# Kernel tuning notes

Measured on AMD Instinct MI355X. Metric: run time of the kernel, lower is better.

The kernel has to match this reference:

```python
import jax, jax.numpy as jnp
import numpy as np

N_NODES = 100000
N_EDGES = 600000
D = 128
NUM_RELS = 200


def setup_inputs() -> dict:
    key = jax.random.key(0)
    ks = jax.random.split(key, 12)
    s = 1.0 / np.sqrt(D)
    return {
        "h": jax.random.normal(ks[0], (N_NODES, D), jnp.float32),
        "prev_h": jax.random.normal(ks[1], (N_NODES, D), jnp.float32),
        "emb_rel": jax.random.normal(ks[2], (NUM_RELS, D), jnp.float32),
        "norm": jax.random.uniform(ks[3], (N_NODES, 1), jnp.float32),
        "weight_neighbor": jax.random.normal(ks[4], (D, D), jnp.float32) * s,
        "loop_weight": jax.random.normal(ks[5], (D, D), jnp.float32) * s,
        "evolve_loop_weight": jax.random.normal(ks[6], (D, D), jnp.float32) * s,
        "skip_connect_weight": jax.random.normal(ks[7], (D, D), jnp.float32) * s,
        "skip_connect_bias": jnp.zeros((D,), jnp.float32),
        "src": jax.random.randint(ks[8], (N_EDGES,), 0, N_NODES, jnp.int64),
        "dst": jax.random.randint(ks[9], (N_EDGES,), 0, N_NODES, jnp.int64),
        "etype": jax.random.randint(ks[10], (N_EDGES,), 0, NUM_RELS, jnp.int64),
    }


def reference(h, prev_h, emb_rel, norm, weight_neighbor, loop_weight,
              evolve_loop_weight, skip_connect_weight, skip_connect_bias,
              src, dst, etype):
    n = h.shape[0]
    # self-loop message: nodes with in-degree > 0 use loop_weight, else evolve_loop_weight
    in_deg = jax.ops.segment_sum(jnp.ones_like(dst, dtype=jnp.float32), dst,
                                 num_segments=n)  # [N]
    loop_message = jnp.where(in_deg[:, None] > 0,
                             h @ loop_weight,
                             h @ evolve_loop_weight)  # [N, D]
    # skip gate from previous layer hidden state
    skip_weight = jax.nn.sigmoid(prev_h @ skip_connect_weight + skip_connect_bias)
    # msg_func: gather src node feats + relation embedding, per-edge GEMM
    msg = (h[src] + emb_rel[etype]) @ weight_neighbor  # [E, D]
    # fn.sum scatter aggregation, then apply_func: multiply by node norm
    agg = jax.ops.segment_sum(msg, dst, num_segments=n)  # [N, D]
    node_repr = agg * norm
    # skip_connect (prev_h non-empty) + self_loop branch
    node_repr = node_repr + loop_message
    node_repr = skip_weight * node_repr + (1.0 - skip_weight) * prev_h
    # activation
    return jax.nn.relu(node_repr)
```

## Files before the change

kernel.cpp:

```cpp
#include <hip/hip_runtime.h>

#define DD 128

typedef __attribute__((ext_vector_type(8))) short short8;
typedef __attribute__((ext_vector_type(4))) float f32x4;
typedef __attribute__((ext_vector_type(4))) int i32x4;

__device__ __forceinline__ unsigned short f2bf(float f) {
    union { float f; unsigned int i; } c; c.f = f;
    unsigned int x = c.i;
    return (unsigned short)((x + 0x7fffu + ((x >> 16) & 1u)) >> 16);
}
__device__ __forceinline__ float bfu(unsigned short u) {
    union { unsigned int i; float f; } c; c.i = ((unsigned int)u) << 16; return c.f;
}
__device__ __forceinline__ void gload_lds16(const void* g, void* l) {
    __builtin_amdgcn_global_load_lds(
        (const __attribute__((address_space(1))) unsigned int*)g,
        (__attribute__((address_space(3))) unsigned int*)l, 16, 0, 0);
}
__device__ __forceinline__ int idx_at(const int* p, int e, int is64) {
    return is64 ? p[2 * e] : p[e];
}
__device__ __forceinline__ int block_is64(const int* dst, int nE, int* s_flag) {
    if (threadIdx.x == 0) *s_flag = 0;
    __syncthreads();
    int w = 2 * (int)threadIdx.x + 1;
    if (threadIdx.x < 128 && w < nE && dst[w] != 0) atomicOr(s_flag, 1);
    __syncthreads();
    return !*s_flag;
}

__global__ __launch_bounds__(256) void prep_k(
    const float* __restrict__ h,
    const float* __restrict__ W0, const float* __restrict__ W1,
    const float* __restrict__ W2, const float* __restrict__ emb,
    const int* __restrict__ dst,
    unsigned short* __restrict__ hB,
    unsigned short* __restrict__ embB, unsigned short* __restrict__ Wt,
    int* __restrict__ deg, int nN, int nEmbEl, int nE) {
    int tid = threadIdx.x;
    int bid = blockIdx.x;
    int nHistB = (nE + 1023) / 1024;
    if (bid < nHistB) {
        __shared__ int s_flag;
        int is64 = block_is64(dst, nE, &s_flag);
        int e0 = bid * 1024 + tid * 4;
        #pragma unroll
        for (int j = 0; j < 4; ++j) {
            int e = e0 + j;
            if (e < nE) atomicAdd(deg + idx_at(dst, e, is64), 1);
        }
        return;
    }
    bid -= nHistB;
    int totalH = nN * DD;
    int nConvH = (totalH + 8191) / 8192;
    if (bid < nConvH) {
        int base0 = bid * 8192;
        if (base0 + 8192 <= totalH) {
            int base = base0 + tid * 8;
            f32x4 x[4][2];
            #pragma unroll
            for (int i = 0; i < 4; ++i) {
                x[i][0] = *(const f32x4*)(h + base + i * 2048);
                x[i][1] = *(const f32x4*)(h + base + i * 2048 + 4);
            }
            #pragma unroll
            for (int i = 0; i < 4; ++i) {
                short8 p;
                #pragma unroll
                for (int j = 0; j < 4; ++j) {
                    p[j]     = (short)f2bf(x[i][0][j]);
                    p[4 + j] = (short)f2bf(x[i][1][j]);
                }
                *(short8*)(hB + base + i * 2048) = p;
            }
        } else {
            #pragma unroll
            for (int i = 0; i < 4; ++i) {
                int b2 = base0 + i * 2048 + tid * 8;
                if (b2 + 8 <= totalH) {
                    f32x4 x0 = *(const f32x4*)(h + b2);
                    f32x4 x1 = *(const f32x4*)(h + b2 + 4);
                    short8 p;
                    #pragma unroll
                    for (int j = 0; j < 4; ++j) {
                        p[j]     = (short)f2bf(x0[j]);
                        p[4 + j] = (short)f2bf(x1[j]);
                    }
                    *(short8*)(hB + b2) = p;
                } else {
                    for (int j = b2; j < totalH && j < b2 + 8; ++j)
                        hB[j] = f2bf(h[j]);
                }
            }
        }
        return;
    }
    bid -= nConvH;
    if (bid < 48) {
        const float* Ws[3] = {W0, W1, W2};
        int w = bid >> 4, chunk = bid & 15;
        unsigned short* T = Wt + w * (DD * DD);
        #pragma unroll
        for (int i = 0; i < 4; ++i) {
            int t = chunk * 1024 + i * 256 + tid;
            int n = t >> 7, k = t & 127;
            T[t] = f2bf(Ws[w][k * DD + n]);
        }
        return;
    }
    bid -= 48;
    int base = bid * 2048 + tid * 8;
    if (base + 8 <= nEmbEl) {
        f32x4 x0 = *(const f32x4*)(emb + base);
        f32x4 x1 = *(const f32x4*)(emb + base + 4);
        short8 p;
        #pragma unroll
        for (int j = 0; j < 4; ++j) {
            p[j]     = (short)f2bf(x0[j]);
            p[4 + j] = (short)f2bf(x1[j]);
        }
        *(short8*)(embB + base) = p;
    } else {
        for (int j = base; j < nEmbEl; ++j) embB[j] = f2bf(emb[j]);
    }
}

__global__ __launch_bounds__(1024) void scan1_k(const int* deg, int* off, int* bsum,
                                                int nN) {
    __shared__ int s[1024];
    int t = threadIdx.x, i = blockIdx.x * 1024 + t;
    int v = (i < nN) ? deg[i] : 0;
    s[t] = v;
    __syncthreads();
    for (int d = 1; d < 1024; d <<= 1) {
        int x = (t >= d) ? s[t - d] : 0;
        __syncthreads();
        s[t] += x;
        __syncthreads();
    }
    if (i < nN) off[i] = s[t] - v;
    if (t == 1023) bsum[blockIdx.x] = s[1023];
}

__global__ __launch_bounds__(1024) void scan23_k(const int* bsum, int* off,
                                                 int* cursor, int nN, int nB) {
    __shared__ int s[1024];
    int t = threadIdx.x;
    s[t] = (t < nB) ? bsum[t] : 0;
    __syncthreads();
    for (int d = 1; d < 1024; d <<= 1) {
        int x = (t >= d) ? s[t - d] : 0;
        __syncthreads();
        s[t] += x;
        __syncthreads();
    }
    int base = (blockIdx.x == 0) ? 0 : s[blockIdx.x - 1];
    int i = blockIdx.x * 1024 + t;
    if (i < nN) {
        int o = off[i] + base;
        off[i] = o;
        cursor[i] = o;
    }
}

__global__ __launch_bounds__(256) void sort_k(const int* src, const int* dst,
                                              const int* et, int nE,
                                              int* cursor, unsigned int* edges) {
    __shared__ int s_flag;
    int is64 = block_is64(dst, nE, &s_flag);
    int e = blockIdx.x * 256 + threadIdx.x;
    if (e >= nE) return;
    int d = idx_at(dst, e, is64);
    int pos = atomicAdd(cursor + d, 1);
    edges[pos] = (unsigned int)idx_at(src, e, is64) |
                 ((unsigned int)idx_at(et, e, is64) << 17);
}

__global__ __launch_bounds__(256) void gather_k(
    const unsigned short* __restrict__ hB, const unsigned short* __restrict__ embB,
    const unsigned int* __restrict__ edges, const int* __restrict__ off,
    const int* __restrict__ deg, const float* __restrict__ normv,
    char* __restrict__ aggP, int nN) {
    int lane = threadIdx.x & 63;
    int v = blockIdx.x * 4 + (threadIdx.x >> 6);
    if (v >= nN) return;
    int slot = lane >> 4, l16 = lane & 15;
    int b = off[v], n = deg[v];
    float a[8] = {0.f, 0.f, 0.f, 0.f, 0.f, 0.f, 0.f, 0.f};
    for (int base = 0; base < n; base += 8) {
        int m0 = base + slot, m1 = base + 4 + slot;
        bool v0 = m0 < n, v1 = m1 < n;
        unsigned int w0 = 0, w1 = 0;
        if (v0) w0 = edges[b + m0];
        if (v1) w1 = edges[b + m1];
        short8 hv0, rv0, hv1, rv1;
        if (v0) {
            hv0 = *(const short8*)(hB + (size_t)(w0 & 0x1FFFFu) * DD + l16 * 8);
            rv0 = *(const short8*)(embB + (size_t)(w0 >> 17) * DD + l16 * 8);
        }
        if (v1) {
            hv1 = *(const short8*)(hB + (size_t)(w1 & 0x1FFFFu) * DD + l16 * 8);
            rv1 = *(const short8*)(embB + (size_t)(w1 >> 17) * DD + l16 * 8);
        }
        if (v0) {
            #pragma unroll
            for (int j = 0; j < 8; ++j)
                a[j] += bfu((unsigned short)hv0[j]) + bfu((unsigned short)rv0[j]);
        }
        if (v1) {
            #pragma unroll
            for (int j = 0; j < 8; ++j)
                a[j] += bfu((unsigned short)hv1[j]) + bfu((unsigned short)rv1[j]);
        }
    }
    #pragma unroll
    for (int j = 0; j < 8; ++j) {
        a[j] += __shfl_xor(a[j], 16);
        a[j] += __shfl_xor(a[j], 32);
    }
    if (slot == 0) {
        float nm = normv[v];
        short8 p;
        #pragma unroll
        for (int j = 0; j < 8; ++j) p[j] = (short)f2bf(a[j] * nm);
        *(short8*)(aggP + (size_t)v * 512 + l16 * 16) = p;
    }
}

__global__ __launch_bounds__(256, 3) void fused_k(
    const unsigned short* __restrict__ hB,
    const float* __restrict__ prevh,
    const float* __restrict__ bias,
    const char* __restrict__ aggP,
    const unsigned short* __restrict__ Wt,
    float* __restrict__ out, int nN) {
    __shared__ unsigned short lds[3 * 64 * 128];
    const int lane = threadIdx.x & 63;
    const int wv = threadIdx.x >> 6;
    const int q = lane >> 4, cl = lane & 15;
    const int node_base = blockIdx.x * 64;
    const int ncb = wv * 32;

    {
        int r0 = lane >> 4;
        int c  = lane & 15;
        #pragma unroll
        for (int it = 0; it < 4; ++it) {
            int r = it * 16 + wv * 4 + r0;
            int row = node_base + r; if (row > nN - 1) row = nN - 1;
            int sw = (c ^ (r & 15)) << 4;
            char* base = (char*)lds + (it * 16 + wv * 4) * 256;
            gload_lds16(aggP + (size_t)row * 512 + sw, base);
            gload_lds16((const char*)hB + (size_t)row * 256 + sw, base + 16384);
        }
    }
    {
        f32x4 t0[4], t1[4];
        #pragma unroll
        for (int it = 0; it < 4; ++it) {
            int pos = it * 512 + lane * 8;
            int row = pos >> 7;
            int col = pos & 127;
            int node = node_base + wv * 16 + row;
            if (node > nN - 1) node = nN - 1;
            const float* g = prevh + (size_t)node * DD + col;
            t0[it] = *(const f32x4*)g;
            t1[it] = *(const f32x4*)(g + 4);
        }
        #pragma unroll
        for (int it = 0; it < 4; ++it) {
            int pos = it * 512 + lane * 8;
            int r = wv * 16 + (pos >> 7);
            int c = (pos & 127) >> 3;
            short8 p;
            #pragma unroll
            for (int j = 0; j < 4; ++j) {
                p[j]     = (short)f2bf(t0[it][j]);
                p[4 + j] = (short)f2bf(t1[it][j]);
            }
            *(short8*)((char*)lds + 32768 + r * 256 + ((c ^ (r & 15)) << 4)) = p;
        }
    }
    __syncthreads();

    const unsigned short* lA = lds;
    const unsigned short* lH = lds + 64 * 128;
    const unsigned short* lP = lds + 2 * 64 * 128;

    f32x4 accM[4][2], accG[4][2];
    #pragma unroll
    for (int mt = 0; mt < 4; ++mt)
        #pragma unroll
        for (int nt = 0; nt < 2; ++nt) {
            accM[mt][nt] = (f32x4){0.f, 0.f, 0.f, 0.f};
            accG[mt][nt] = (f32x4){0.f, 0.f, 0.f, 0.f};
        }

    #pragma unroll
    for (int ks = 0; ks < 4; ++ks) {
        short8 bn[2], bl[2], bs[2];
        #pragma unroll
        for (int nt = 0; nt < 2; ++nt) {
            int n = (ncb + nt * 16 + cl) * DD + ks * 32 + q * 8;
            bn[nt] = *(const short8*)(Wt + n);
            bl[nt] = *(const short8*)(Wt + DD * DD + n);
            bs[nt] = *(const short8*)(Wt + 2 * DD * DD + n);
        }
        int swz = ((ks * 4 + q) ^ cl) << 3;
        #pragma unroll
        for (int mt = 0; mt < 4; ++mt) {
            int off = (mt * 16 + cl) * 128 + swz;
            short8 aA = *(const short8*)(lA + off);
            short8 aH = *(const short8*)(lH + off);
            short8 aP = *(const short8*)(lP + off);
            #pragma unroll
            for (int nt = 0; nt < 2; ++nt) {
                accM[mt][nt] = __builtin_amdgcn_mfma_f32_16x16x32_bf16(
                    aA, bn[nt], accM[mt][nt], 0, 0, 0);
                accM[mt][nt] = __builtin_amdgcn_mfma_f32_16x16x32_bf16(
                    aH, bl[nt], accM[mt][nt], 0, 0, 0);
                accG[mt][nt] = __builtin_amdgcn_mfma_f32_16x16x32_bf16(
                    aP, bs[nt], accG[mt][nt], 0, 0, 0);
            }
        }
    }

    float b0 = bias[ncb + cl], b1 = bias[ncb + 16 + cl];

    #pragma unroll
    for (int mt = 0; mt < 4; ++mt) {
        #pragma unroll
        for (int r = 0; r < 4; ++r) {
            int nrow = mt * 16 + q * 4 + r;
            int node = node_base + nrow;
            if (node >= nN) continue;
            #pragma unroll
            for (int nt = 0; nt < 2; ++nt) {
                int col = ncb + nt * 16 + cl;
                float pv = bfu(lP[nrow * 128 +
                                  ((((col >> 3) ^ (nrow & 15)) << 3) | (col & 7))]);
                float sg = 1.0f / (1.0f + __expf(-(accG[mt][nt][r] + (nt ? b1 : b0))));
                float o  = sg * accM[mt][nt][r] + (1.0f - sg) * pv;
                out[(size_t)node * DD + col] = (o > 0.f ? o : 0.f);
            }
        }
    }
}

__global__ __launch_bounds__(256) void fix_k(
    const float* __restrict__ h, const float* __restrict__ prevh,
    const float* __restrict__ bias, const float* __restrict__ We,
    const float* __restrict__ Wsk, const int* __restrict__ deg,
    float* __restrict__ out, int nN, int chunk) {
    __shared__ int list[256];
    __shared__ int cnt;
    __shared__ float hrow[DD], prow[DD], res[2][DD];
    int tid = threadIdx.x;
    int base = blockIdx.x * chunk;
    for (int c = base; c < base + chunk && c < nN; c += 256) {
        if (tid == 0) cnt = 0;
        __syncthreads();
        int v = c + tid;
        if (v < nN && v < base + chunk && deg[v] == 0)
            list[atomicAdd(&cnt, 1)] = v;
        __syncthreads();
        int m = cnt;
        for (int i = 0; i < m; ++i) {
            int node = list[i];
            if (tid < DD) hrow[tid] = h[(size_t)node * DD + tid];
            else prow[tid - DD] = prevh[(size_t)node * DD + tid - DD];
            __syncthreads();
            int col = tid & (DD - 1);
            int half = tid >> 7;
            const float* W = half ? Wsk : We;
            const float* x = half ? prow : hrow;
            float s = 0.f;
            for (int k = 0; k < DD; ++k) s += x[k] * W[k * DD + col];
            res[half][col] = s;
            __syncthreads();
            if (tid < DD) {
                float sg = 1.0f / (1.0f + __expf(-(res[1][col] + bias[col])));
                float o  = sg * res[0][col] + (1.0f - sg) * prow[col];
                out[(size_t)node * DD + col] = (o > 0.f ? o : 0.f);
            }
            __syncthreads();
        }
        __syncthreads();
    }
}

extern "C" void kernel_launch(void* const* d_in, const int* in_sizes, int n_in,
                              void* d_out, int out_size, void* d_ws, size_t ws_size,
                              hipStream_t stream) {
    const float* h     = (const float*)d_in[0];
    const float* prevh = (const float*)d_in[1];
    const float* emb   = (const float*)d_in[2];
    const float* normv = (const float*)d_in[3];
    const float* Wn    = (const float*)d_in[4];
    const float* Wl    = (const float*)d_in[5];
    const float* We    = (const float*)d_in[6];
    const float* Wsk   = (const float*)d_in[7];
    const float* bias  = (const float*)d_in[8];
    const int* src   = (const int*)d_in[9];
    const int* dst   = (const int*)d_in[10];
    const int* etype = (const int*)d_in[11];

    int nN = in_sizes[3];
    int nE = in_sizes[9];
    int nEmbEl = in_sizes[2];

    char* w = (char*)d_ws;
    size_t o = 0;
    unsigned short* Wt = (unsigned short*)(w + o);  o += 3 * DD * DD * 2;
    unsigned short* embB = (unsigned short*)(w + o); o += ((size_t)nEmbEl * 2 + 255) & ~(size_t)255;
    int* deg    = (int*)(w + o);  o += ((size_t)nN * 4 + 15) & ~(size_t)15;
    int* offA   = (int*)(w + o);  o += ((size_t)nN * 4 + 15) & ~(size_t)15;
    int* cursor = (int*)(w + o);  o += ((size_t)nN * 4 + 15) & ~(size_t)15;
    int* bsum   = (int*)(w + o);  o += 4096;
    unsigned int* edges = (unsigned int*)(w + o); o += ((size_t)nE * 4 + 15) & ~(size_t)15;
    unsigned short* hB = (unsigned short*)(w + o);

    int totalH = nN * DD;
    int nConvH = (totalH + 8191) / 8192;
    int nEmbB  = (nEmbEl + 2047) / 2048;
    int nHistB = (nE + 1023) / 1024;
    int nB = (nN + 1023) / 1024;

    hipMemsetAsync(deg, 0, (size_t)nN * sizeof(int), stream);
    prep_k<<<nHistB + nConvH + 48 + nEmbB, 256, 0, stream>>>(
        h, Wn, Wl, Wsk, emb, dst, hB, embB, Wt, deg, nN, nEmbEl, nE);
    scan1_k<<<nB, 1024, 0, stream>>>(deg, offA, bsum, nN);
    scan23_k<<<nB, 1024, 0, stream>>>(bsum, offA, cursor, nN, nB);
    sort_k<<<(nE + 255) / 256, 256, 0, stream>>>(src, dst, etype, nE, cursor, edges);
    gather_k<<<(nN + 3) / 4, 256, 0, stream>>>(hB, embB, edges, offA, deg, normv,
                                               (char*)d_out, nN);
    fused_k<<<(nN + 63) / 64, 256, 0, stream>>>(hB, prevh, bias, (const char*)d_out,
                                                Wt, (float*)d_out, nN);
    int fgrid = 256;
    int chunk = ((nN + fgrid * 256 - 1) / (fgrid * 256)) * 256;
    fix_k<<<fgrid, 256, 0, stream>>>(h, prevh, bias, We, Wsk, deg, (float*)d_out,
                                     nN, chunk);
    (void)ws_size; (void)n_in; (void)out_size;
}
```

Measured before the change: 318.0 us.

## Make fused GEMM kernel persistent with double-buffered LDS tile prefetch

Turns fused_k into a persistent kernel that loops over 64-node tiles with a grid capped at 256 blocks. While one tile is computed, the next tile's agg, h and prev_h data is loaded into a second LDS buffer. The three bf16 weight fragments and the bias are now loaded into registers once per block instead of per tile. The goal is to hide global-load latency and drop the repeated weight loads, at the cost of one block (four waves) per CU, 96 KB of dynamic LDS, and much higher register pressure.

```diff
diff --git a/kernel.cpp b/kernel.cpp
--- a/kernel.cpp
+++ b/kernel.cpp
@@ -230,45 +230,58 @@
     }
 }
 
-__global__ __launch_bounds__(256, 3) void fused_k(
+__global__ __launch_bounds__(256, 1) void fused_k(
     const unsigned short* __restrict__ hB,
     const float* __restrict__ prevh,
     const float* __restrict__ bias,
     const char* __restrict__ aggP,
     const unsigned short* __restrict__ Wt,
-    float* __restrict__ out, int nN) {
-    __shared__ unsigned short lds[3 * 64 * 128];
+    float* __restrict__ out, int nN, int nTiles) {
+    extern __shared__ unsigned short lds[];
     const int lane = threadIdx.x & 63;
     const int wv = threadIdx.x >> 6;
     const int q = lane >> 4, cl = lane & 15;
-    const int node_base = blockIdx.x * 64;
     const int ncb = wv * 32;
+    const int stride = gridDim.x;
+
+    int t = blockIdx.x;
+    if (t >= nTiles) return;
+
+    short8 bn[4][2], bl[4][2], bs[4][2];
+    #pragma unroll
+    for (int ks = 0; ks < 4; ++ks)
+        #pragma unroll
+        for (int nt = 0; nt < 2; ++nt) {
+            int n = (ncb + nt * 16 + cl) * DD + ks * 32 + q * 8;
+            bn[ks][nt] = *(const short8*)(Wt + n);
+            bl[ks][nt] = *(const short8*)(Wt + DD * DD + n);
+            bs[ks][nt] = *(const short8*)(Wt + 2 * DD * DD + n);
+        }
+    const float b0 = bias[ncb + cl], b1 = bias[ncb + 16 + cl];
+
+    const int r0 = lane >> 4;
+    const int c16 = lane & 15;
 
     {
-        int r0 = lane >> 4;
-        int c  = lane & 15;
+        int node_base = t * 64;
         #pragma unroll
         for (int it = 0; it < 4; ++it) {
             int r = it * 16 + wv * 4 + r0;
             int row = node_base + r; if (row > nN - 1) row = nN - 1;
-            int sw = (c ^ (r & 15)) << 4;
-            char* base = (char*)lds + (it * 16 + wv * 4) * 256;
-            gload_lds16(aggP + (size_t)row * 512 + sw, base);
-            gload_lds16((const char*)hB + (size_t)row * 256 + sw, base + 16384);
-        }
-    }
-    {
-        f32x4 t0[4], t1[4];
+            int sw = (c16 ^ (r & 15)) << 4;
+            char* bptr = (char*)lds + (it * 16 + wv * 4) * 256;
+            gload_lds16(aggP + (size_t)row * 512 + sw, bptr);
+            gload_lds16((const char*)hB + (size_t)row * 256 + sw, bptr + 16384);
+        }
+        f32x4 p0[4], p1[4];
         #pragma unroll
         for (int it = 0; it < 4; ++it) {
             int pos = it * 512 + lane * 8;
-            int row = pos >> 7;
-            int col = pos & 127;
-            int node = node_base + wv * 16 + row;
+            int node = node_base + wv * 16 + (pos >> 7);
             if (node > nN - 1) node = nN - 1;
-            const float* g = prevh + (size_t)node * DD + col;
-            t0[it] = *(const f32x4*)g;
-            t1[it] = *(const f32x4*)(g + 4);
+            const float* g = prevh + (size_t)node * DD + (pos & 127);
+            p0[it] = *(const f32x4*)g;
+            p1[it] = *(const f32x4*)(g + 4);
         }
         #pragma unroll
         for (int it = 0; it < 4; ++it) {
@@ -278,75 +291,117 @@
             short8 p;
             #pragma unroll
             for (int j = 0; j < 4; ++j) {
-                p[j]     = (short)f2bf(t0[it][j]);
-                p[4 + j] = (short)f2bf(t1[it][j]);
+                p[j]     = (short)f2bf(p0[it][j]);
+                p[4 + j] = (short)f2bf(p1[it][j]);
             }
             *(short8*)((char*)lds + 32768 + r * 256 + ((c ^ (r & 15)) << 4)) = p;
         }
     }
     __syncthreads();
 
-    const unsigned short* lA = lds;
-    const unsigned short* lH = lds + 64 * 128;
-    const unsigned short* lP = lds + 2 * 64 * 128;
-
-    f32x4 accM[4][2], accG[4][2];
-    #pragma unroll
-    for (int mt = 0; mt < 4; ++mt)
-        #pragma unroll
-        for (int nt = 0; nt < 2; ++nt) {
-            accM[mt][nt] = (f32x4){0.f, 0.f, 0.f, 0.f};
-            accG[mt][nt] = (f32x4){0.f, 0.f, 0.f, 0.f};
-        }
-
-    #pragma unroll
-    for (int ks = 0; ks < 4; ++ks) {
-        short8 bn[2], bl[2], bs[2];
-        #pragma unroll
-        for (int nt = 0; nt < 2; ++nt) {
-            int n = (ncb + nt * 16 + cl) * DD + ks * 32 + q * 8;
-            bn[nt] = *(const short8*)(Wt + n);
-            bl[nt] = *(const short8*)(Wt + DD * DD + n);
-            bs[nt] = *(const short8*)(Wt + 2 * DD * DD + n);
-        }
-        int swz = ((ks * 4 + q) ^ cl) << 3;
+    int cur = 0;
+    for (;;) {
+        int node_base = t * 64;
+        int tn = t + stride;
+        bool more = (tn < nTiles);
+
+        f32x4 p0[4], p1[4];
+        if (more) {
+            int nb2 = tn * 64;
+            char* dbuf = (char*)lds + (cur ^ 1) * 49152;
+            #pragma unroll
+            for (int it = 0; it < 4; ++it) {
+                int r = it * 16 + wv * 4 + r0;
+                int row = nb2 + r; if (row > nN - 1) row = nN - 1;
+                int sw = (c16 ^ (r & 15)) << 4;
+                char* bptr = dbuf + (it * 16 + wv * 4) * 256;
+                gload_lds16(aggP + (size_t)row * 512 + sw, bptr);
+                gload_lds16((const char*)hB + (size_t)row * 256 + sw, bptr + 16384);
+            }
+            #pragma unroll
+            for (int it = 0; it < 4; ++it) {
+                int pos = it * 512 + lane * 8;
+                int node = nb2 + wv * 16 + (pos >> 7);
+                if (node > nN - 1) node = nN - 1;
+                const float* g = prevh + (size_t)node * DD + (pos & 127);
+                p0[it] = *(const f32x4*)g;
+                p1[it] = *(const f32x4*)(g + 4);
+            }
+        }
+
+        const unsigned short* lA = lds + cur * 24576;
+        const unsigned short* lH = lA + 8192;
+        const unsigned short* lP = lA + 16384;
+
+        f32x4 accM[4][2], accG[4][2];
+        #pragma unroll
+        for (int mt = 0; mt < 4; ++mt)
+            #pragma unroll
+            for (int nt = 0; nt < 2; ++nt) {
+                accM[mt][nt] = (f32x4){0.f, 0.f, 0.f, 0.f};
+                accG[mt][nt] = (f32x4){0.f, 0.f, 0.f, 0.f};
+            }
+        #pragma unroll
+        for (int ks = 0; ks < 4; ++ks) {
+            int swz = ((ks * 4 + q) ^ cl) << 3;
+            #pragma unroll
+            for (int mt = 0; mt < 4; ++mt) {
+                int off = (mt * 16 + cl) * 128 + swz;
+                short8 aA = *(const short8*)(lA + off);
+                short8 aH = *(const short8*)(lH + off);
+                short8 aP = *(const short8*)(lP + off);
+                #pragma unroll
+                for (int nt = 0; nt < 2; ++nt) {
+                    accM[mt][nt] = __builtin_amdgcn_mfma_f32_16x16x32_bf16(
+                        aA, bn[ks][nt], accM[mt][nt], 0, 0, 0);
+                    accM[mt][nt] = __builtin_amdgcn_mfma_f32_16x16x32_bf16(
+                        aH, bl[ks][nt], accM[mt][nt], 0, 0, 0);
+                    accG[mt][nt] = __builtin_amdgcn_mfma_f32_16x16x32_bf16(
+                        aP, bs[ks][nt], accG[mt][nt], 0, 0, 0);
+                }
+            }
+        }
+
         #pragma unroll
         for (int mt = 0; mt < 4; ++mt) {
-            int off = (mt * 16 + cl) * 128 + swz;
-            short8 aA = *(const short8*)(lA + off);
-            short8 aH = *(const short8*)(lH + off);
-            short8 aP = *(const short8*)(lP + off);
-            #pragma unroll
-            for (int nt = 0; nt < 2; ++nt) {
-                accM[mt][nt] = __builtin_amdgcn_mfma_f32_16x16x32_bf16(
-                    aA, bn[nt], accM[mt][nt], 0, 0, 0);
-                accM[mt][nt] = __builtin_amdgcn_mfma_f32_16x16x32_bf16(
-                    aH, bl[nt], accM[mt][nt], 0, 0, 0);
-                accG[mt][nt] = __builtin_amdgcn_mfma_f32_16x16x32_bf16(
-                    aP, bs[nt], accG[mt][nt], 0, 0, 0);
-            }
-        }
-    }
-
-    float b0 = bias[ncb + cl], b1 = bias[ncb + 16 + cl];
-
-    #pragma unroll
-    for (int mt = 0; mt < 4; ++mt) {
-        #pragma unroll
-        for (int r = 0; r < 4; ++r) {
-            int nrow = mt * 16 + q * 4 + r;
-            int node = node_base + nrow;
-            if (node >= nN) continue;
-            #pragma unroll
-            for (int nt = 0; nt < 2; ++nt) {
-                int col = ncb + nt * 16 + cl;
-                float pv = bfu(lP[nrow * 128 +
-                                  ((((col >> 3) ^ (nrow & 15)) << 3) | (col & 7))]);
-                float sg = 1.0f / (1.0f + __expf(-(accG[mt][nt][r] + (nt ? b1 : b0))));
-                float o  = sg * accM[mt][nt][r] + (1.0f - sg) * pv;
-                out[(size_t)node * DD + col] = (o > 0.f ? o : 0.f);
-            }
-        }
+            #pragma unroll
+            for (int r = 0; r < 4; ++r) {
+                int nrow = mt * 16 + q * 4 + r;
+                int node = node_base + nrow;
+                if (node >= nN) continue;
+                #pragma unroll
+                for (int nt = 0; nt < 2; ++nt) {
+                    int col = ncb + nt * 16 + cl;
+                    float pv = bfu(lP[nrow * 128 +
+                                      ((((col >> 3) ^ (nrow & 15)) << 3) | (col & 7))]);
+                    float sg = 1.0f / (1.0f + __expf(-(accG[mt][nt][r] +
+                                                       (nt ? b1 : b0))));
+                    float o  = sg * accM[mt][nt][r] + (1.0f - sg) * pv;
+                    out[(size_t)node * DD + col] = (o > 0.f ? o : 0.f);
+                }
+            }
+        }
+
+        if (more) {
+            char* dbuf = (char*)lds + (cur ^ 1) * 49152;
+            #pragma unroll
+            for (int it = 0; it < 4; ++it) {
+                int pos = it * 512 + lane * 8;
+                int r = wv * 16 + (pos >> 7);
+                int c = (pos & 127) >> 3;
+                short8 p;
+                #pragma unroll
+                for (int j = 0; j < 4; ++j) {
+                    p[j]     = (short)f2bf(p0[it][j]);
+                    p[4 + j] = (short)f2bf(p1[it][j]);
+                }
+                *(short8*)(dbuf + 32768 + r * 256 + ((c ^ (r & 15)) << 4)) = p;
+            }
+        }
+        __syncthreads();
+        if (!more) break;
+        cur ^= 1;
+        t = tn;
     }
 }
 
@@ -428,6 +483,8 @@
     int nEmbB  = (nEmbEl + 2047) / 2048;
     int nHistB = (nE + 1023) / 1024;
     int nB = (nN + 1023) / 1024;
+    int nTiles = (nN + 63) / 64;
+    int fgrid2 = nTiles < 256 ? nTiles : 256;
 
     hipMemsetAsync(deg, 0, (size_t)nN * sizeof(int), stream);
     prep_k<<<nHistB + nConvH + 48 + nEmbB, 256, 0, stream>>>(
@@ -437,8 +494,8 @@
     sort_k<<<(nE + 255) / 256, 256, 0, stream>>>(src, dst, etype, nE, cursor, edges);
     gather_k<<<(nN + 3) / 4, 256, 0, stream>>>(hB, embB, edges, offA, deg, normv,
                                                (char*)d_out, nN);
-    fused_k<<<(nN + 63) / 64, 256, 0, stream>>>(hB, prevh, bias, (const char*)d_out,
-                                                Wt, (float*)d_out, nN);
+    fused_k<<<fgrid2, 256, 98304, stream>>>(hB, prevh, bias, (const char*)d_out,
+                                            Wt, (float*)d_out, nN, nTiles);
     int fgrid = 256;
     int chunk = ((nN + fgrid * 256 - 1) / (fgrid * 256)) * 256;
     fix_k<<<fgrid, 256, 0, stream>>>(h, prevh, bias, We, Wsk, deg, (float*)d_out,
```

Result: no change. 311.8 us (-1.9%).
